# Kernel optimization log

Hardware: AMD Instinct MI355X
Metric: run time of the kernel (lower is better)

Reference implementation:

```python
import jax, jax.numpy as jnp
import numpy as np

N = 50000    # nodes
E = 600000   # edges
H = 128      # hidden_dim
NF = 12      # n_features
L = 4        # n_layers
EPS = 1e-5   # LayerNorm eps


def setup_inputs() -> dict:
    key = jax.random.key(0)
    ks = jax.random.split(key, 32)

    def w(k, shape, fan_in):
        return (jax.random.normal(k, shape, jnp.float32) / np.float32(np.sqrt(fan_in)))

    inp = {
        "x": jax.random.normal(ks[0], (N, NF), jnp.float32),
        "edge_index": jax.random.randint(ks[1], (2, E), 0, N, dtype=jnp.int64),
        # encoder: Linear(NF,H) -> ReLU -> Linear(H,H)
        "enc_W1": w(ks[2], (NF, H), NF), "enc_b1": jnp.zeros((H,), jnp.float32),
        "enc_W2": w(ks[3], (H, H), H),   "enc_b2": jnp.zeros((H,), jnp.float32),
        # L residual SAGE blocks (PyG SAGEConv: lin_l on mean-aggr w/ bias, lin_r on self no bias)
        "lin_l_W": w(ks[4], (L, H, H), H), "lin_l_b": jnp.zeros((L, H), jnp.float32),
        "lin_r_W": w(ks[5], (L, H, H), H),
        "ln_g": jnp.ones((L, H), jnp.float32), "ln_b": jnp.zeros((L, H), jnp.float32),
        # disp head: H->H->H//2->3
        "dW1": w(ks[6], (H, H), H),      "db1": jnp.zeros((H,), jnp.float32),
        "dW2": w(ks[7], (H, H // 2), H), "db2": jnp.zeros((H // 2,), jnp.float32),
        "dW3": w(ks[8], (H // 2, 3), H // 2), "db3": jnp.zeros((3,), jnp.float32),
        # stress head: H->H->H//2->1
        "sW1": w(ks[9], (H, H), H),       "sb1": jnp.zeros((H,), jnp.float32),
        "sW2": w(ks[10], (H, H // 2), H), "sb2": jnp.zeros((H // 2,), jnp.float32),
        "sW3": w(ks[11], (H // 2, 1), H // 2), "sb3": jnp.zeros((1,), jnp.float32),
    }
    return inp


def reference(x, edge_index, enc_W1, enc_b1, enc_W2, enc_b2,
              lin_l_W, lin_l_b, lin_r_W, ln_g, ln_b,
              dW1, db1, dW2, db2, dW3, db3,
              sW1, sb1, sW2, sb2, sW3, sb3):
    src, dst = edge_index[0], edge_index[1]

    # linear load-scaling ratio from load columns [3:6]
    load_mag = jnp.linalg.norm(x[:, 3:6], axis=1)
    ratio = jnp.max(load_mag)

    # encoder MLP
    h = jnp.maximum(x @ enc_W1 + enc_b1, 0.0) @ enc_W2 + enc_b2  # [N, H]

    # in-degree for mean aggregation (clamped to 1 like PyG)
    deg = jax.ops.segment_sum(jnp.ones((E,), h.dtype), dst, num_segments=N)
    inv_deg = 1.0 / jnp.clip(deg, 1.0)[:, None]  # [N, 1]

    for l in range(L):
        # SAGEConv: mean of neighbor (src) features at dst, then lin_l(aggr) + lin_r(self)
        agg = jax.ops.segment_sum(h[src], dst, num_segments=N) * inv_deg  # [N, H]
        y = agg @ lin_l_W[l] + lin_l_b[l] + h @ lin_r_W[l]
        # LayerNorm over channels
        mu = jnp.mean(y, axis=-1, keepdims=True)
        var = jnp.var(y, axis=-1, keepdims=True)
        y = (y - mu) * jax.lax.rsqrt(var + EPS) * ln_g[l] + ln_b[l]
        # residual + ReLU
        h = h + jnp.maximum(y, 0.0)

    # heads
    d = jnp.maximum(h @ dW1 + db1, 0.0)
    d = jnp.maximum(d @ dW2 + db2, 0.0) @ dW3 + db3  # [N, 3]
    s = jnp.maximum(h @ sW1 + sb1, 0.0)
    s = jnp.maximum(s @ sW2 + sb2, 0.0) @ sW3 + sb3  # [N, 1]

    # linear_scaling = True
    d = d * ratio
    s = s * ratio
    return jnp.concatenate([d, s], axis=1)  # [N, 4]
```

## Files before the change

kernel.cpp:

```cpp
#include <hip/hip_runtime.h>
#include <hip/hip_bf16.h>

typedef __hip_bfloat16 bf16;
typedef short bf16x8 __attribute__((ext_vector_type(8)));
typedef float f32x4 __attribute__((ext_vector_type(4)));

__device__ __forceinline__ float2 bfpair(unsigned u){
  float2 r; r.x = __uint_as_float(u<<16); r.y = __uint_as_float(u & 0xffff0000u); return r;
}
__device__ __forceinline__ float bfu(unsigned short u){ return __uint_as_float(((unsigned)u)<<16); }
__device__ __forceinline__ unsigned f2bf(float f){
  unsigned u = __float_as_uint(f);
  return (u + 0x7fffu + ((u>>16)&1u)) >> 16;
}
__device__ __forceinline__ unsigned fpack(float a, float b){
  return (f2bf(b)<<16) | f2bf(a);
}
__device__ __forceinline__ int edge_is64(const int* e){
  return (e[1]==0) & (e[3]==0) & (e[5]==0);
}
__device__ __forceinline__ int edge_ld(const int* e, int is64, int idx){
  return e[is64 ? 2*idx : idx];
}

__global__ void k_pre(const float* __restrict__ x, const int* __restrict__ eidx,
                      unsigned* __restrict__ ratio, int* __restrict__ deg,
                      int N, int E, int nbE,
                      const float* __restrict__ llW, const float* __restrict__ lrW,
                      const float* __restrict__ dW1, const float* __restrict__ sW1,
                      const float* __restrict__ dW2, const float* __restrict__ sW2,
                      const float* __restrict__ eW2,
                      unsigned short* __restrict__ WTs, unsigned short* __restrict__ WT1,
                      unsigned short* __restrict__ WT2, unsigned short* __restrict__ WE2){
  int b = (int)blockIdx.x;
  if(b < nbE){
    int e = b*256 + threadIdx.x;
    if(e>=E) return;
    int is64 = edge_is64(eidx);
    int d = edge_ld(eidx, is64, E+e);
    if((unsigned)d < (unsigned)N) atomicAdd(&deg[d], 1);
    return;
  }
  if(b < nbE + 256){
    int i = (b-nbE)*256 + threadIdx.x;
    int stride = 256*256;
    float m = 0.f;
    for(; i<N; i+=stride){
      float a = x[(size_t)i*12+3];
      float bb = x[(size_t)i*12+4];
      float c = x[(size_t)i*12+5];
      m = fmaxf(m, sqrtf(a*a+bb*bb+c*c));
    }
    #pragma unroll
    for(int off=1; off<64; off<<=1) m = fmaxf(m, __shfl_xor(m, off));
    if((threadIdx.x & 63)==0) atomicMax(ratio, __float_as_uint(m));
    return;
  }
  int idx = (b - nbE - 256)*256 + threadIdx.x;
  int j = idx & 7;
  int lane = (idx>>3) & 63;
  int q = lane >> 4, p = lane & 15;
  if(idx < 131072){
    int nt = (idx>>9) & 7, ks = (idx>>12) & 7, l = (idx>>15) & 3;
    int k = ks*32 + q*8 + j, n = nt*16 + p;
    float v = (k<128) ? llW[(size_t)l*16384 + (size_t)k*128 + n]
                      : lrW[(size_t)l*16384 + (size_t)(k-128)*128 + n];
    WTs[idx] = (unsigned short)f2bf(v);
  } else if(idx < 163840){
    int i2 = idx - 131072;
    int nt = (i2>>9) & 15, ks = (i2>>13) & 3;
    int k = ks*32 + q*8 + j, n = nt*16 + p;
    float v = (n<128) ? dW1[(size_t)k*128 + n] : sW1[(size_t)k*128 + (n-128)];
    WT1[i2] = (unsigned short)f2bf(v);
  } else if(idx < 180224){
    int i2 = idx - 163840;
    int nt = (i2>>9) & 7, ks = (i2>>12) & 3;
    int k = ks*32 + q*8 + j, n = nt*16 + p;
    float v = (n<64) ? dW2[(size_t)k*64 + n] : sW2[(size_t)k*64 + (n-64)];
    WT2[i2] = (unsigned short)f2bf(v);
  } else if(idx < 196608){
    int i2 = idx - 180224;
    int nt = (i2>>9) & 7, ks = (i2>>12) & 3;
    int k = ks*32 + q*8 + j, n = nt*16 + p;
    WE2[i2] = (unsigned short)f2bf(eW2[(size_t)k*128 + n]);
  }
}

__global__ void k_scan1(const int* __restrict__ deg, int* __restrict__ bsum, int N){
  int t = threadIdx.x;
  int idx0 = blockIdx.x*1024 + t*4;
  int s=0;
  #pragma unroll
  for(int i=0;i<4;i++){ int idx=idx0+i; if(idx<N) s += deg[idx]; }
  #pragma unroll
  for(int off=1; off<64; off<<=1) s += __shfl_xor(s, off);
  __shared__ int ws4[4];
  if((t&63)==0) ws4[t>>6]=s;
  __syncthreads();
  if(t==0) bsum[blockIdx.x]=ws4[0]+ws4[1]+ws4[2]+ws4[3];
}
__global__ void k_scan3(const int* __restrict__ deg, const int* __restrict__ bsum,
                        int* __restrict__ offs, int* __restrict__ pos,
                        float* __restrict__ invdeg, int N, int E, int nb){
  __shared__ int sb[64];
  int t = threadIdx.x;
  if(t < 64){
    int v = (t<nb)? bsum[t] : 0;
    int incl = v;
    #pragma unroll
    for(int off=1; off<64; off<<=1){ int u = __shfl_up(incl, (unsigned)off); if(t>=off) incl+=u; }
    sb[t] = incl - v;
  }
  __syncthreads();
  int idx0 = blockIdx.x*1024 + t*4;
  int d[4]; int s=0;
  #pragma unroll
  for(int i=0;i<4;i++){ int idx=idx0+i; d[i] = (idx<N)? deg[idx]:0; s+=d[i]; }
  int lane=t&63, w=t>>6;
  int incl=s;
  #pragma unroll
  for(int off=1; off<64; off<<=1){ int v=__shfl_up(incl, (unsigned)off); if(lane>=off) incl+=v; }
  __shared__ int wsum[4];
  if(lane==63) wsum[w]=incl;
  __syncthreads();
  int base = sb[blockIdx.x];
  for(int i=0;i<w;i++) base += wsum[i];
  int run = base + incl - s;
  #pragma unroll
  for(int i=0;i<4;i++){
    int idx=idx0+i;
    if(idx<N){
      offs[idx]=run; pos[idx]=run;
      invdeg[idx] = 1.0f / (float)(d[i]>0? d[i]:1);
    }
    run += d[i];
  }
  if(blockIdx.x==0 && t==0) offs[N]=E;
}

__global__ void k_bucket(const int* __restrict__ eidx, int* __restrict__ pos,
                         int* __restrict__ csr, int E, int N){
  int e = blockIdx.x*blockDim.x + threadIdx.x;
  if(e>=E) return;
  int is64 = edge_is64(eidx);
  int d = edge_ld(eidx, is64, E+e);
  int s = edge_ld(eidx, is64, e);
  if((unsigned)d >= (unsigned)N) return;
  if((unsigned)s >= (unsigned)N) s = 0;
  int p = atomicAdd(&pos[d], 1);
  if((unsigned)p < (unsigned)E) csr[p] = s;
}

__global__ __launch_bounds__(256) void k_encoder(
  const float* __restrict__ x,
  const float* __restrict__ W1, const float* __restrict__ b1,
  const unsigned short* __restrict__ WE2, const float* __restrict__ b2,
  bf16* __restrict__ h, int N)
{
  __shared__ float Xs[64][12];
  __shared__ float W1s[12][128];
  __shared__ float b1s[128];
  __shared__ __align__(16) unsigned short T1b[64][136];
  int tid = threadIdx.x;
  int tx = tid & 31, ty = tid >> 5;
  int rowBase = blockIdx.x*64;
  for(int idx=tid; idx<768; idx+=256){
    int r = idx/12, c = idx - r*12;
    int row = rowBase + r;
    Xs[r][c] = (row<N)? x[(size_t)row*12+c] : 0.f;
  }
  for(int idx=tid; idx<1536; idx+=256) W1s[idx>>7][idx&127] = W1[idx];
  if(tid<128) b1s[tid] = b1[tid];
  __syncthreads();
  float acc[8][4] = {};
  #pragma unroll
  for(int k=0;k<12;k++){
    float4 w4 = *(float4*)&W1s[k][tx*4];
    #pragma unroll
    for(int r=0;r<8;r++){
      float a = Xs[ty*8+r][k];
      acc[r][0]+=a*w4.x; acc[r][1]+=a*w4.y; acc[r][2]+=a*w4.z; acc[r][3]+=a*w4.w;
    }
  }
  #pragma unroll
  for(int r=0;r<8;r++)
    #pragma unroll
    for(int c=0;c<4;c++)
      T1b[ty*8+r][tx*4+c] = (unsigned short)f2bf(fmaxf(acc[r][c] + b1s[tx*4+c], 0.f));
  __syncthreads();

  int lane = tid & 63;
  int w = tid >> 6, q = lane >> 4, p = lane & 15;
  f32x4 acc2[8];
  #pragma unroll
  for(int nt=0; nt<8; nt++) acc2[nt] = (f32x4){0.f,0.f,0.f,0.f};
  #pragma unroll
  for(int ks=0; ks<4; ks++){
    bf16x8 af = *(const bf16x8*)&T1b[w*16+p][ks*32+q*8];
    #pragma unroll
    for(int nt=0; nt<8; nt++){
      bf16x8 bfr = *(const bf16x8*)(WE2 + ((size_t)(ks*8+nt)*64 + lane)*8);
      acc2[nt] = __builtin_amdgcn_mfma_f32_16x16x32_bf16(af, bfr, acc2[nt], 0,0,0);
    }
  }
  float b2v[8];
  #pragma unroll
  for(int nt=0; nt<8; nt++) b2v[nt] = b2[nt*16+p];
  unsigned short* hu = (unsigned short*)h;
  #pragma unroll
  for(int r=0;r<4;r++){
    int row = rowBase + w*16 + q*4 + r;
    if(row < N){
      #pragma unroll
      for(int nt=0; nt<8; nt++)
        hu[(size_t)row*128 + nt*16+p] = (unsigned short)f2bf(acc2[nt][r] + b2v[nt]);
    }
  }
}

__global__ __launch_bounds__(256) void k_layer16(
    const bf16* __restrict__ hin, bf16* __restrict__ hout,
    const int* __restrict__ offs, const int* __restrict__ csr,
    const float* __restrict__ invdeg,
    const unsigned short* __restrict__ WT,
    const float* __restrict__ bl, const float* __restrict__ lng,
    const float* __restrict__ lnb, int N, int E)
{
  __shared__ __align__(16) unsigned short Ag[16][136];
  __shared__ float sPart[4][16];
  __shared__ float qPart[4][16];
  int tid = threadIdx.x;
  int rowBase = blockIdx.x*16;

  {
    int qw = tid >> 4;
    int l  = tid & 15;
    int row = rowBase + qw;
    float a0=0.f,a1=0.f,a2=0.f,a3=0.f,a4=0.f,a5=0.f,a6=0.f,a7=0.f;
    if(row < N){
      int s = offs[row], e = offs[row+1];
      s = max(0, min(s, E)); e = max(s, min(e, E));
      int i = s;
      for(; i+4<=e; i+=4){
        int j0=csr[i], j1=csr[i+1], j2=csr[i+2], j3=csr[i+3];
        uint4 u0 = *(const uint4*)(hin + (size_t)j0*128 + l*8);
        uint4 u1 = *(const uint4*)(hin + (size_t)j1*128 + l*8);
        uint4 u2 = *(const uint4*)(hin + (size_t)j2*128 + l*8);
        uint4 u3 = *(const uint4*)(hin + (size_t)j3*128 + l*8);
        float2 f;
        f=bfpair(u0.x); a0+=f.x; a1+=f.y;  f=bfpair(u0.y); a2+=f.x; a3+=f.y;
        f=bfpair(u0.z); a4+=f.x; a5+=f.y;  f=bfpair(u0.w); a6+=f.x; a7+=f.y;
        f=bfpair(u1.x); a0+=f.x; a1+=f.y;  f=bfpair(u1.y); a2+=f.x; a3+=f.y;
        f=bfpair(u1.z); a4+=f.x; a5+=f.y;  f=bfpair(u1.w); a6+=f.x; a7+=f.y;
        f=bfpair(u2.x); a0+=f.x; a1+=f.y;  f=bfpair(u2.y); a2+=f.x; a3+=f.y;
        f=bfpair(u2.z); a4+=f.x; a5+=f.y;  f=bfpair(u2.w); a6+=f.x; a7+=f.y;
        f=bfpair(u3.x); a0+=f.x; a1+=f.y;  f=bfpair(u3.y); a2+=f.x; a3+=f.y;
        f=bfpair(u3.z); a4+=f.x; a5+=f.y;  f=bfpair(u3.w); a6+=f.x; a7+=f.y;
      }
      for(; i<e; ++i){
        int jj = csr[i];
        uint4 u = *(const uint4*)(hin + (size_t)jj*128 + l*8);
        float2 f;
        f=bfpair(u.x); a0+=f.x; a1+=f.y;  f=bfpair(u.y); a2+=f.x; a3+=f.y;
        f=bfpair(u.z); a4+=f.x; a5+=f.y;  f=bfpair(u.w); a6+=f.x; a7+=f.y;
      }
      float id = invdeg[row];
      a0*=id; a1*=id; a2*=id; a3*=id; a4*=id; a5*=id; a6*=id; a7*=id;
    }
    uint4 o;
    o.x = fpack(a0,a1); o.y = fpack(a2,a3);
    o.z = fpack(a4,a5); o.w = fpack(a6,a7);
    *(uint4*)&Ag[qw][l*8] = o;
  }
  __syncthreads();

  int lane = tid & 63;
  int w = tid >> 6;
  int q = lane >> 4;
  int p = lane & 15;
  int nt0 = 2*w, nt1 = 2*w+1;
  int am = rowBase + p;
  bool ok = am < N;
  const unsigned short* hRow = (const unsigned short*)hin + (size_t)am*128;

  f32x4 accA = (f32x4){0.f,0.f,0.f,0.f};
  f32x4 accB = (f32x4){0.f,0.f,0.f,0.f};
  #pragma unroll
  for(int ks=0; ks<8; ks++){
    bf16x8 af;
    if(ks < 4){
      af = *(const bf16x8*)&Ag[p][ks*32 + q*8];
    } else {
      af = (bf16x8){0,0,0,0,0,0,0,0};
      if(ok) af = *(const bf16x8*)(hRow + (ks-4)*32 + q*8);
    }
    bf16x8 b0 = *(const bf16x8*)(WT + ((size_t)(ks*8+nt0)*64 + lane)*8);
    bf16x8 b1 = *(const bf16x8*)(WT + ((size_t)(ks*8+nt1)*64 + lane)*8);
    accA = __builtin_amdgcn_mfma_f32_16x16x32_bf16(af, b0, accA, 0,0,0);
    accB = __builtin_amdgcn_mfma_f32_16x16x32_bf16(af, b1, accB, 0,0,0);
  }

  int c0 = nt0*16 + p, c1 = nt1*16 + p;
  float bl0 = bl[c0], g0 = lng[c0], lb0 = lnb[c0];
  float bl1 = bl[c1], g1 = lng[c1], lb1 = lnb[c1];
  float y0[4], y1[4];
  #pragma unroll
  for(int r=0;r<4;r++){
    y0[r] = accA[r] + bl0;
    y1[r] = accB[r] + bl1;
    float s  = y0[r] + y1[r];
    float sq = y0[r]*y0[r] + y1[r]*y1[r];
    #pragma unroll
    for(int off=1; off<16; off<<=1){ s += __shfl_xor(s, off); sq += __shfl_xor(sq, off); }
    if(p==0){ sPart[w][q*4+r] = s; qPart[w][q*4+r] = sq; }
  }
  __syncthreads();

  const unsigned short* hiu = (const unsigned short*)hin;
  unsigned short* hou = (unsigned short*)hout;
  #pragma unroll
  for(int r=0;r<4;r++){
    int rloc = q*4 + r;
    float s  = sPart[0][rloc]+sPart[1][rloc]+sPart[2][rloc]+sPart[3][rloc];
    float sq = qPart[0][rloc]+qPart[1][rloc]+qPart[2][rloc]+qPart[3][rloc];
    float mu = s*(1.f/128.f);
    float var = fmaxf(sq*(1.f/128.f) - mu*mu, 0.f);
    float rstd = rsqrtf(var + 1e-5f);
    int row = rowBase + rloc;
    if(row < N){
      float h0 = bfu(hiu[(size_t)row*128 + c0]);
      float h1 = bfu(hiu[(size_t)row*128 + c1]);
      float o0 = h0 + fmaxf((y0[r]-mu)*rstd*g0 + lb0, 0.f);
      float o1 = h1 + fmaxf((y1[r]-mu)*rstd*g1 + lb1, 0.f);
      hou[(size_t)row*128 + c0] = (unsigned short)f2bf(o0);
      hou[(size_t)row*128 + c1] = (unsigned short)f2bf(o1);
    }
  }
}

__global__ __launch_bounds__(256) void k_heads_mfma(
  const bf16* __restrict__ h,
  const unsigned short* __restrict__ WT1,
  const unsigned short* __restrict__ WT2,
  const float* __restrict__ db1, const float* __restrict__ sb1,
  const float* __restrict__ db2, const float* __restrict__ sb2,
  const float* __restrict__ dW3, const float* __restrict__ db3,
  const float* __restrict__ sW3, const float* __restrict__ sb3,
  const float* __restrict__ ratio_p, float* __restrict__ out, int N)
{
  __shared__ __align__(16) unsigned short T1s[4][16][264];
  const float ratio = *ratio_p;
  int tid = threadIdx.x;
  int lane = tid & 63;
  int w = tid >> 6;
  int q = lane >> 4;
  int p = lane & 15;
  int rowBase = blockIdx.x*64;
  int am = rowBase + w*16 + p;
  bool arow_ok = am < N;
  const unsigned short* hRow = (const unsigned short*)h + (size_t)am*128;

  f32x4 acc1[16];
  #pragma unroll
  for(int nt=0; nt<16; nt++) acc1[nt] = (f32x4){0.f,0.f,0.f,0.f};
  #pragma unroll
  for(int ks=0; ks<4; ks++){
    int koff = ks*32 + q*8;
    bf16x8 af = {0,0,0,0,0,0,0,0};
    if(arow_ok) af = *(const bf16x8*)(hRow + koff);
    #pragma unroll
    for(int nt=0; nt<16; nt++){
      bf16x8 bfr = *(const bf16x8*)(WT1 + ((size_t)(ks*16+nt)*64 + lane)*8);
      acc1[nt] = __builtin_amdgcn_mfma_f32_16x16x32_bf16(af, bfr, acc1[nt], 0,0,0);
    }
  }
  #pragma unroll
  for(int nt=0; nt<16; nt++){
    float b1v = (nt<8) ? db1[nt*16+p] : sb1[(nt-8)*16+p];
    #pragma unroll
    for(int r=0;r<4;r++){
      float v = fmaxf(acc1[nt][r] + b1v, 0.f);
      T1s[w][q*4+r][nt*16+p] = (unsigned short)f2bf(v);
    }
  }
  __syncthreads();

  f32x4 acc2[8];
  #pragma unroll
  for(int nt=0; nt<8; nt++) acc2[nt] = (f32x4){0.f,0.f,0.f,0.f};
  #pragma unroll
  for(int ks=0; ks<4; ks++){
    int koff = ks*32 + q*8;
    bf16x8 ad = *(const bf16x8*)&T1s[w][p][koff];
    bf16x8 as = *(const bf16x8*)&T1s[w][p][128+koff];
    #pragma unroll
    for(int nt=0; nt<8; nt++){
      bf16x8 bfr = *(const bf16x8*)(WT2 + ((size_t)(ks*8+nt)*64 + lane)*8);
      acc2[nt] = __builtin_amdgcn_mfma_f32_16x16x32_bf16(nt<4? ad : as, bfr, acc2[nt], 0,0,0);
    }
  }

  float w3d[4][3], w3s[4], bd2[4], bs2[4];
  #pragma unroll
  for(int nt=0; nt<4; nt++){
    #pragma unroll
    for(int c=0;c<3;c++) w3d[nt][c] = dW3[(nt*16+p)*3 + c];
    w3s[nt] = sW3[nt*16+p];
    bd2[nt] = db2[nt*16+p];
    bs2[nt] = sb2[nt*16+p];
  }
  float b3v = (p==0)? db3[0] : (p==1)? db3[1] : (p==2)? db3[2] : sb3[0];
  #pragma unroll
  for(int r=0;r<4;r++){
    int row = rowBase + w*16 + q*4 + r;
    float pd0=0.f, pd1=0.f, pd2=0.f, ps=0.f;
    #pragma unroll
    for(int nt=0; nt<4; nt++){
      float td = fmaxf(acc2[nt][r]   + bd2[nt], 0.f);
      float ts = fmaxf(acc2[nt+4][r] + bs2[nt], 0.f);
      pd0 += td*w3d[nt][0]; pd1 += td*w3d[nt][1]; pd2 += td*w3d[nt][2];
      ps  += ts*w3s[nt];
    }
    #pragma unroll
    for(int off=1; off<16; off<<=1){
      pd0 += __shfl_xor(pd0, off); pd1 += __shfl_xor(pd1, off);
      pd2 += __shfl_xor(pd2, off); ps  += __shfl_xor(ps, off);
    }
    if(row < N && p < 4){
      float v = (p==0)? pd0 : (p==1)? pd1 : (p==2)? pd2 : ps;
      out[(size_t)row*4 + p] = (v + b3v)*ratio;
    }
  }
}

extern "C" void kernel_launch(void* const* d_in, const int* in_sizes, int n_in,
                              void* d_out, int out_size, void* d_ws, size_t ws_size,
                              hipStream_t stream)
{
  const float* x   = (const float*)d_in[0];
  const int*  eidx = (const int*) d_in[1];
  const float* eW1 = (const float*)d_in[2];
  const float* eb1 = (const float*)d_in[3];
  const float* eW2 = (const float*)d_in[4];
  const float* eb2 = (const float*)d_in[5];
  const float* llW = (const float*)d_in[6];
  const float* llb = (const float*)d_in[7];
  const float* lrW = (const float*)d_in[8];
  const float* lng = (const float*)d_in[9];
  const float* lnb = (const float*)d_in[10];
  const float* dW1 = (const float*)d_in[11];
  const float* db1 = (const float*)d_in[12];
  const float* dW2 = (const float*)d_in[13];
  const float* db2 = (const float*)d_in[14];
  const float* dW3 = (const float*)d_in[15];
  const float* db3 = (const float*)d_in[16];
  const float* sW1 = (const float*)d_in[17];
  const float* sb1 = (const float*)d_in[18];
  const float* sW2 = (const float*)d_in[19];
  const float* sb2 = (const float*)d_in[20];
  const float* sW3 = (const float*)d_in[21];
  const float* sb3 = (const float*)d_in[22];
  float* out = (float*)d_out;

  const int N = in_sizes[0] / 12;
  const int E = in_sizes[1] / 2;
  (void)n_in; (void)out_size; (void)ws_size;

  char* base = (char*)d_ws;
  size_t off = 0;
  auto alloc = [&](size_t nbytes)->char*{
    char* p = base + off; off += (nbytes + 255) & ~(size_t)255; return p;
  };
  unsigned* ratio = (unsigned*)alloc(4);
  int*   deg    = (int*)  alloc((size_t)N*4);
  int*   offs   = (int*)  alloc(((size_t)N+1)*4);
  int*   pos    = (int*)  alloc((size_t)N*4);
  int*   bsum   = (int*)  alloc(256*4);
  int*   csr    = (int*)  alloc((size_t)E*4);
  float* invdeg = (float*)alloc((size_t)N*4);
  bf16*  hA     = (bf16*) alloc((size_t)N*128*2);
  bf16*  hB     = (bf16*) alloc((size_t)N*128*2);
  unsigned short* WTs  = (unsigned short*)alloc((size_t)131072*2);
  unsigned short* WT1h = (unsigned short*)alloc((size_t)32768*2);
  unsigned short* WT2h = (unsigned short*)alloc((size_t)16384*2);
  unsigned short* WE2  = (unsigned short*)alloc((size_t)16384*2);

  size_t zbytes = (size_t)((char*)offs - base);
  hipMemsetAsync(d_ws, 0, zbytes, stream);

  int nbE    = (E + 255)/256;
  int nbScan = (N + 1023)/1024;
  int nbTile = (N + 63)/64;
  int nbLay  = (N + 15)/16;

  k_pre  <<<nbE + 256 + 768, 256, 0, stream>>>(x, eidx, ratio, deg, N, E, nbE,
      llW, lrW, dW1, sW1, dW2, sW2, eW2, WTs, WT1h, WT2h, WE2);
  k_scan1<<<nbScan, 256, 0, stream>>>(deg, bsum, N);
  k_scan3<<<nbScan, 256, 0, stream>>>(deg, bsum, offs, pos, invdeg, N, E, nbScan);
  k_bucket<<<nbE, 256, 0, stream>>>(eidx, pos, csr, E, N);

  k_encoder<<<nbTile, 256, 0, stream>>>(x, eW1, eb1, WE2, eb2, hA, N);
  bf16* hin = hA; bf16* hout = hB;
  for(int l=0;l<4;l++){
    k_layer16<<<nbLay, 256, 0, stream>>>(hin, hout, offs, csr, invdeg,
        WTs + (size_t)l*32768,
        llb + (size_t)l*128, lng + (size_t)l*128, lnb + (size_t)l*128, N, E);
    bf16* t = hin; hin = hout; hout = t;
  }
  k_heads_mfma<<<nbTile, 256, 0, stream>>>(hin, WT1h, WT2h,
      db1, sb1, db2, sb2, dW3, db3, sW3, sb3, (const float*)ratio, out, N);
}
```

Measured before the change: 353.4 us.

## Merge encoder with CSR bucketing and widen SAGE layer tile to 32 rows

The encoder and the CSR bucketing kernel now run as one launch, split by block index, so the two independent stages can overlap and one launch is saved. Each SAGE layer block now processes 32 rows instead of 16. Each wave runs two M-tiles of MFMA that share the same weight fragments, which halves weight reloads per row and halves the grid size. The cost is more registers per thread, fewer blocks to hide gather latency, and a serial two-row gather loop per thread.

```diff
diff --git a/kernel.cpp b/kernel.cpp
--- a/kernel.cpp
+++ b/kernel.cpp
@@ -138,25 +138,25 @@
   if(blockIdx.x==0 && t==0) offs[N]=E;
 }
 
-__global__ void k_bucket(const int* __restrict__ eidx, int* __restrict__ pos,
-                         int* __restrict__ csr, int E, int N){
-  int e = blockIdx.x*blockDim.x + threadIdx.x;
-  if(e>=E) return;
-  int is64 = edge_is64(eidx);
-  int d = edge_ld(eidx, is64, E+e);
-  int s = edge_ld(eidx, is64, e);
-  if((unsigned)d >= (unsigned)N) return;
-  if((unsigned)s >= (unsigned)N) s = 0;
-  int p = atomicAdd(&pos[d], 1);
-  if((unsigned)p < (unsigned)E) csr[p] = s;
-}
-
-__global__ __launch_bounds__(256) void k_encoder(
+__global__ __launch_bounds__(256) void k_enc_bucket(
   const float* __restrict__ x,
   const float* __restrict__ W1, const float* __restrict__ b1,
   const unsigned short* __restrict__ WE2, const float* __restrict__ b2,
-  bf16* __restrict__ h, int N)
+  bf16* __restrict__ h, int N, int nbTile,
+  const int* __restrict__ eidx, int* __restrict__ pos, int* __restrict__ csr, int E)
 {
+  if((int)blockIdx.x >= nbTile){
+    int e = ((int)blockIdx.x - nbTile)*256 + threadIdx.x;
+    if(e>=E) return;
+    int is64 = edge_is64(eidx);
+    int d = edge_ld(eidx, is64, E+e);
+    int s = edge_ld(eidx, is64, e);
+    if((unsigned)d >= (unsigned)N) return;
+    if((unsigned)s >= (unsigned)N) s = 0;
+    int p = atomicAdd(&pos[d], 1);
+    if((unsigned)p < (unsigned)E) csr[p] = s;
+    return;
+  }
   __shared__ float Xs[64][12];
   __shared__ float W1s[12][128];
   __shared__ float b1s[128];
@@ -218,7 +218,7 @@
   }
 }
 
-__global__ __launch_bounds__(256) void k_layer16(
+__global__ __launch_bounds__(256) void k_layer32(
     const bf16* __restrict__ hin, bf16* __restrict__ hout,
     const int* __restrict__ offs, const int* __restrict__ csr,
     const float* __restrict__ invdeg,
@@ -226,51 +226,55 @@
     const float* __restrict__ bl, const float* __restrict__ lng,
     const float* __restrict__ lnb, int N, int E)
 {
-  __shared__ __align__(16) unsigned short Ag[16][136];
-  __shared__ float sPart[4][16];
-  __shared__ float qPart[4][16];
+  __shared__ __align__(16) unsigned short Ag[32][136];
+  __shared__ float sPart[4][32];
+  __shared__ float qPart[4][32];
   int tid = threadIdx.x;
-  int rowBase = blockIdx.x*16;
+  int rowBase = blockIdx.x*32;
 
   {
     int qw = tid >> 4;
     int l  = tid & 15;
-    int row = rowBase + qw;
-    float a0=0.f,a1=0.f,a2=0.f,a3=0.f,a4=0.f,a5=0.f,a6=0.f,a7=0.f;
-    if(row < N){
-      int s = offs[row], e = offs[row+1];
-      s = max(0, min(s, E)); e = max(s, min(e, E));
-      int i = s;
-      for(; i+4<=e; i+=4){
-        int j0=csr[i], j1=csr[i+1], j2=csr[i+2], j3=csr[i+3];
-        uint4 u0 = *(const uint4*)(hin + (size_t)j0*128 + l*8);
-        uint4 u1 = *(const uint4*)(hin + (size_t)j1*128 + l*8);
-        uint4 u2 = *(const uint4*)(hin + (size_t)j2*128 + l*8);
-        uint4 u3 = *(const uint4*)(hin + (size_t)j3*128 + l*8);
-        float2 f;
-        f=bfpair(u0.x); a0+=f.x; a1+=f.y;  f=bfpair(u0.y); a2+=f.x; a3+=f.y;
-        f=bfpair(u0.z); a4+=f.x; a5+=f.y;  f=bfpair(u0.w); a6+=f.x; a7+=f.y;
-        f=bfpair(u1.x); a0+=f.x; a1+=f.y;  f=bfpair(u1.y); a2+=f.x; a3+=f.y;
-        f=bfpair(u1.z); a4+=f.x; a5+=f.y;  f=bfpair(u1.w); a6+=f.x; a7+=f.y;
-        f=bfpair(u2.x); a0+=f.x; a1+=f.y;  f=bfpair(u2.y); a2+=f.x; a3+=f.y;
-        f=bfpair(u2.z); a4+=f.x; a5+=f.y;  f=bfpair(u2.w); a6+=f.x; a7+=f.y;
-        f=bfpair(u3.x); a0+=f.x; a1+=f.y;  f=bfpair(u3.y); a2+=f.x; a3+=f.y;
-        f=bfpair(u3.z); a4+=f.x; a5+=f.y;  f=bfpair(u3.w); a6+=f.x; a7+=f.y;
+    #pragma unroll
+    for(int rr=0; rr<2; rr++){
+      int rloc = qw + rr*16;
+      int row = rowBase + rloc;
+      float a0=0.f,a1=0.f,a2=0.f,a3=0.f,a4=0.f,a5=0.f,a6=0.f,a7=0.f;
+      if(row < N){
+        int s = offs[row], e = offs[row+1];
+        s = max(0, min(s, E)); e = max(s, min(e, E));
+        int i = s;
+        for(; i+4<=e; i+=4){
+          int j0=csr[i], j1=csr[i+1], j2=csr[i+2], j3=csr[i+3];
+          uint4 u0 = *(const uint4*)(hin + (size_t)j0*128 + l*8);
+          uint4 u1 = *(const uint4*)(hin + (size_t)j1*128 + l*8);
+          uint4 u2 = *(const uint4*)(hin + (size_t)j2*128 + l*8);
+          uint4 u3 = *(const uint4*)(hin + (size_t)j3*128 + l*8);
+          float2 f;
+          f=bfpair(u0.x); a0+=f.x; a1+=f.y;  f=bfpair(u0.y); a2+=f.x; a3+=f.y;
+          f=bfpair(u0.z); a4+=f.x; a5+=f.y;  f=bfpair(u0.w); a6+=f.x; a7+=f.y;
+          f=bfpair(u1.x); a0+=f.x; a1+=f.y;  f=bfpair(u1.y); a2+=f.x; a3+=f.y;
+          f=bfpair(u1.z); a4+=f.x; a5+=f.y;  f=bfpair(u1.w); a6+=f.x; a7+=f.y;
+          f=bfpair(u2.x); a0+=f.x; a1+=f.y;  f=bfpair(u2.y); a2+=f.x; a3+=f.y;
+          f=bfpair(u2.z); a4+=f.x; a5+=f.y;  f=bfpair(u2.w); a6+=f.x; a7+=f.y;
+          f=bfpair(u3.x); a0+=f.x; a1+=f.y;  f=bfpair(u3.y); a2+=f.x; a3+=f.y;
+          f=bfpair(u3.z); a4+=f.x; a5+=f.y;  f=bfpair(u3.w); a6+=f.x; a7+=f.y;
+        }
+        for(; i<e; ++i){
+          int jj = csr[i];
+          uint4 u = *(const uint4*)(hin + (size_t)jj*128 + l*8);
+          float2 f;
+          f=bfpair(u.x); a0+=f.x; a1+=f.y;  f=bfpair(u.y); a2+=f.x; a3+=f.y;
+          f=bfpair(u.z); a4+=f.x; a5+=f.y;  f=bfpair(u.w); a6+=f.x; a7+=f.y;
+        }
+        float id = invdeg[row];
+        a0*=id; a1*=id; a2*=id; a3*=id; a4*=id; a5*=id; a6*=id; a7*=id;
       }
-      for(; i<e; ++i){
-        int jj = csr[i];
-        uint4 u = *(const uint4*)(hin + (size_t)jj*128 + l*8);
-        float2 f;
-        f=bfpair(u.x); a0+=f.x; a1+=f.y;  f=bfpair(u.y); a2+=f.x; a3+=f.y;
-        f=bfpair(u.z); a4+=f.x; a5+=f.y;  f=bfpair(u.w); a6+=f.x; a7+=f.y;
-      }
-      float id = invdeg[row];
-      a0*=id; a1*=id; a2*=id; a3*=id; a4*=id; a5*=id; a6*=id; a7*=id;
-    }
-    uint4 o;
-    o.x = fpack(a0,a1); o.y = fpack(a2,a3);
-    o.z = fpack(a4,a5); o.w = fpack(a6,a7);
-    *(uint4*)&Ag[qw][l*8] = o;
+      uint4 o;
+      o.x = fpack(a0,a1); o.y = fpack(a2,a3);
+      o.z = fpack(a4,a5); o.w = fpack(a6,a7);
+      *(uint4*)&Ag[rloc][l*8] = o;
+    }
   }
   __syncthreads();
 
@@ -279,61 +283,83 @@
   int q = lane >> 4;
   int p = lane & 15;
   int nt0 = 2*w, nt1 = 2*w+1;
-  int am = rowBase + p;
-  bool ok = am < N;
-  const unsigned short* hRow = (const unsigned short*)hin + (size_t)am*128;
-
-  f32x4 accA = (f32x4){0.f,0.f,0.f,0.f};
-  f32x4 accB = (f32x4){0.f,0.f,0.f,0.f};
+  int am0 = rowBase + p;
+  int am1 = rowBase + 16 + p;
+  bool ok0 = am0 < N, ok1 = am1 < N;
+  const unsigned short* hRow0 = (const unsigned short*)hin + (size_t)am0*128;
+  const unsigned short* hRow1 = (const unsigned short*)hin + (size_t)am1*128;
+
+  f32x4 a00 = (f32x4){0.f,0.f,0.f,0.f};
+  f32x4 a01 = (f32x4){0.f,0.f,0.f,0.f};
+  f32x4 a10 = (f32x4){0.f,0.f,0.f,0.f};
+  f32x4 a11 = (f32x4){0.f,0.f,0.f,0.f};
   #pragma unroll
   for(int ks=0; ks<8; ks++){
-    bf16x8 af;
+    bf16x8 af0, af1;
     if(ks < 4){
-      af = *(const bf16x8*)&Ag[p][ks*32 + q*8];
+      af0 = *(const bf16x8*)&Ag[p][ks*32 + q*8];
+      af1 = *(const bf16x8*)&Ag[16+p][ks*32 + q*8];
     } else {
-      af = (bf16x8){0,0,0,0,0,0,0,0};
-      if(ok) af = *(const bf16x8*)(hRow + (ks-4)*32 + q*8);
+      af0 = (bf16x8){0,0,0,0,0,0,0,0};
+      af1 = (bf16x8){0,0,0,0,0,0,0,0};
+      if(ok0) af0 = *(const bf16x8*)(hRow0 + (ks-4)*32 + q*8);
+      if(ok1) af1 = *(const bf16x8*)(hRow1 + (ks-4)*32 + q*8);
     }
     bf16x8 b0 = *(const bf16x8*)(WT + ((size_t)(ks*8+nt0)*64 + lane)*8);
     bf16x8 b1 = *(const bf16x8*)(WT + ((size_t)(ks*8+nt1)*64 + lane)*8);
-    accA = __builtin_amdgcn_mfma_f32_16x16x32_bf16(af, b0, accA, 0,0,0);
-    accB = __builtin_amdgcn_mfma_f32_16x16x32_bf16(af, b1, accB, 0,0,0);
+    a00 = __builtin_amdgcn_mfma_f32_16x16x32_bf16(af0, b0, a00, 0,0,0);
+    a01 = __builtin_amdgcn_mfma_f32_16x16x32_bf16(af0, b1, a01, 0,0,0);
+    a10 = __builtin_amdgcn_mfma_f32_16x16x32_bf16(af1, b0, a10, 0,0,0);
+    a11 = __builtin_amdgcn_mfma_f32_16x16x32_bf16(af1, b1, a11, 0,0,0);
   }
 
   int c0 = nt0*16 + p, c1 = nt1*16 + p;
   float bl0 = bl[c0], g0 = lng[c0], lb0 = lnb[c0];
   float bl1 = bl[c1], g1 = lng[c1], lb1 = lnb[c1];
-  float y0[4], y1[4];
+  float y00[4], y01[4], y10[4], y11[4];
   #pragma unroll
   for(int r=0;r<4;r++){
-    y0[r] = accA[r] + bl0;
-    y1[r] = accB[r] + bl1;
-    float s  = y0[r] + y1[r];
-    float sq = y0[r]*y0[r] + y1[r]*y1[r];
-    #pragma unroll
-    for(int off=1; off<16; off<<=1){ s += __shfl_xor(s, off); sq += __shfl_xor(sq, off); }
-    if(p==0){ sPart[w][q*4+r] = s; qPart[w][q*4+r] = sq; }
+    y00[r] = a00[r] + bl0;  y01[r] = a01[r] + bl1;
+    y10[r] = a10[r] + bl0;  y11[r] = a11[r] + bl1;
+    float s0  = y00[r] + y01[r];
+    float sq0 = y00[r]*y00[r] + y01[r]*y01[r];
+    float s1  = y10[r] + y11[r];
+    float sq1 = y10[r]*y10[r] + y11[r]*y11[r];
+    #pragma unroll
+    for(int off=1; off<16; off<<=1){
+      s0 += __shfl_xor(s0, off); sq0 += __shfl_xor(sq0, off);
+      s1 += __shfl_xor(s1, off); sq1 += __shfl_xor(sq1, off);
+    }
+    if(p==0){
+      sPart[w][q*4+r] = s0;     qPart[w][q*4+r] = sq0;
+      sPart[w][16+q*4+r] = s1;  qPart[w][16+q*4+r] = sq1;
+    }
   }
   __syncthreads();
 
   const unsigned short* hiu = (const unsigned short*)hin;
   unsigned short* hou = (unsigned short*)hout;
   #pragma unroll
-  for(int r=0;r<4;r++){
-    int rloc = q*4 + r;
-    float s  = sPart[0][rloc]+sPart[1][rloc]+sPart[2][rloc]+sPart[3][rloc];
-    float sq = qPart[0][rloc]+qPart[1][rloc]+qPart[2][rloc]+qPart[3][rloc];
-    float mu = s*(1.f/128.f);
-    float var = fmaxf(sq*(1.f/128.f) - mu*mu, 0.f);
-    float rstd = rsqrtf(var + 1e-5f);
-    int row = rowBase + rloc;
-    if(row < N){
-      float h0 = bfu(hiu[(size_t)row*128 + c0]);
-      float h1 = bfu(hiu[(size_t)row*128 + c1]);
-      float o0 = h0 + fmaxf((y0[r]-mu)*rstd*g0 + lb0, 0.f);
-      float o1 = h1 + fmaxf((y1[r]-mu)*rstd*g1 + lb1, 0.f);
-      hou[(size_t)row*128 + c0] = (unsigned short)f2bf(o0);
-      hou[(size_t)row*128 + c1] = (unsigned short)f2bf(o1);
+  for(int mt=0; mt<2; mt++){
+    #pragma unroll
+    for(int r=0;r<4;r++){
+      int rloc = mt*16 + q*4 + r;
+      float s  = sPart[0][rloc]+sPart[1][rloc]+sPart[2][rloc]+sPart[3][rloc];
+      float sq = qPart[0][rloc]+qPart[1][rloc]+qPart[2][rloc]+qPart[3][rloc];
+      float mu = s*(1.f/128.f);
+      float var = fmaxf(sq*(1.f/128.f) - mu*mu, 0.f);
+      float rstd = rsqrtf(var + 1e-5f);
+      int row = rowBase + rloc;
+      if(row < N){
+        float yv0 = mt ? y10[r] : y00[r];
+        float yv1 = mt ? y11[r] : y01[r];
+        float h0 = bfu(hiu[(size_t)row*128 + c0]);
+        float h1 = bfu(hiu[(size_t)row*128 + c1]);
+        float o0 = h0 + fmaxf((yv0-mu)*rstd*g0 + lb0, 0.f);
+        float o1 = h1 + fmaxf((yv1-mu)*rstd*g1 + lb1, 0.f);
+        hou[(size_t)row*128 + c0] = (unsigned short)f2bf(o0);
+        hou[(size_t)row*128 + c1] = (unsigned short)f2bf(o1);
+      }
     }
   }
 }
@@ -491,18 +517,18 @@
   int nbE    = (E + 255)/256;
   int nbScan = (N + 1023)/1024;
   int nbTile = (N + 63)/64;
-  int nbLay  = (N + 15)/16;
+  int nbLay  = (N + 31)/32;
 
   k_pre  <<<nbE + 256 + 768, 256, 0, stream>>>(x, eidx, ratio, deg, N, E, nbE,
       llW, lrW, dW1, sW1, dW2, sW2, eW2, WTs, WT1h, WT2h, WE2);
   k_scan1<<<nbScan, 256, 0, stream>>>(deg, bsum, N);
   k_scan3<<<nbScan, 256, 0, stream>>>(deg, bsum, offs, pos, invdeg, N, E, nbScan);
-  k_bucket<<<nbE, 256, 0, stream>>>(eidx, pos, csr, E, N);
-
-  k_encoder<<<nbTile, 256, 0, stream>>>(x, eW1, eb1, WE2, eb2, hA, N);
+  k_enc_bucket<<<nbTile + nbE, 256, 0, stream>>>(x, eW1, eb1, WE2, eb2, hA, N, nbTile,
+      eidx, pos, csr, E);
+
   bf16* hin = hA; bf16* hout = hB;
   for(int l=0;l<4;l++){
-    k_layer16<<<nbLay, 256, 0, stream>>>(hin, hout, offs, csr, invdeg,
+    k_layer32<<<nbLay, 256, 0, stream>>>(hin, hout, offs, csr, invdeg,
         WTs + (size_t)l*32768,
         llb + (size_t)l*128, lng + (size_t)l*128, lnb + (size_t)l*128, N, E);
     bf16* t = hin; hin = hout; hout = t;
```

After: 381.9 us. 8.1% more time.
